# Optimization experiments

Hardware: AMD Instinct MI355X
Metric: run time of the kernel (lower is better)

## Reference

```python
import jax, jax.numpy as jnp
import numpy as np

H = 8        # num attention heads
DH = 160     # head dim (hidden_size // H)
HS = 1280    # hidden_size
CAD = 768    # cross_attention_dim
R = 4        # LoRA rank
LORA_SCALE = 1.0  # `scale` forward arg (default 1.0)


def setup_inputs() -> dict:
    key = jax.random.key(0)
    ks = jax.random.split(key, 16)
    rn = lambda k, s, std=0.02: (jax.random.normal(k, s) * std).astype(jnp.float32)
    return {
        "hidden_states": jax.random.normal(ks[0], (8, 4096, HS), jnp.float32),
        "encoder_hidden_states": jax.random.normal(ks[1], (8, 77, CAD), jnp.float32),
        # base attention projections (nn.Linear weight layout: [out, in])
        "Wq": rn(ks[2], (HS, HS)),
        "Wk": rn(ks[3], (HS, CAD)),
        "Wv": rn(ks[4], (HS, CAD)),
        "Wo": rn(ks[5], (HS, HS)),
        "bo": jnp.zeros((HS,), jnp.float32),
        # LoRA down/up pairs (down std ~ 1/rank; up nonzero so grads flow)
        "q_down": rn(ks[6], (R, HS), 0.25), "q_up": rn(ks[7], (HS, R)),
        "k_down": rn(ks[8], (R, CAD), 0.25), "k_up": rn(ks[9], (HS, R)),
        "v_down": rn(ks[10], (R, CAD), 0.25), "v_up": rn(ks[11], (HS, R)),
        "o_down": rn(ks[12], (R, HS), 0.25), "o_up": rn(ks[13], (HS, R)),
    }


def reference(hidden_states, encoder_hidden_states, Wq, Wk, Wv, Wo, bo,
              q_down, q_up, k_down, k_up, v_down, v_up, o_down, o_up):
    B, S, _ = hidden_states.shape
    T = encoder_hidden_states.shape[1]
    lora = lambda x, d, u: (x @ d.T) @ u.T  # LoRALinearLayer: up(down(x))

    q = hidden_states @ Wq.T + LORA_SCALE * lora(hidden_states, q_down, q_up)
    k = encoder_hidden_states @ Wk.T + LORA_SCALE * lora(encoder_hidden_states, k_down, k_up)
    v = encoder_hidden_states @ Wv.T + LORA_SCALE * lora(encoder_hidden_states, v_down, v_up)

    q = q.reshape(B, S, H, DH)
    k = k.reshape(B, T, H, DH)
    v = v.reshape(B, T, H, DH)

    # attn.get_attention_scores: scaled QK^T, softmax (no mask)
    inv_sqrt_d = jnp.asarray(1.0 / np.sqrt(DH), q.dtype)
    scores = jnp.einsum('bshd,bthd->bhst', q, k) * inv_sqrt_d
    probs = jax.nn.softmax(scores, axis=-1)
    o = jnp.einsum('bhst,bthd->bshd', probs, v).reshape(B, S, H * DH)

    # to_out[0] (Linear with bias) + LoRA on the same input; to_out[1] dropout = identity (eval)
    return o @ Wo.T + bo + LORA_SCALE * lora(o, o_down, o_up)
```

## Files before the change

### kernel.cpp

```cpp
#include <hip/hip_runtime.h>
#include <hip/hip_bf16.h>
#include <stdint.h>

typedef short bf16x8 __attribute__((ext_vector_type(8)));
typedef float f32x4 __attribute__((ext_vector_type(4)));

#define DEVI static __device__ __forceinline__

DEVI ushort f2bf(float f) {
  union { float f; uint32_t u; } v; v.f = f;
  uint32_t u = v.u;
  return (ushort)((u + 0x7fffu + ((u >> 16) & 1u)) >> 16);
}

DEVI void gload16(const void* g, void* l) {
  __builtin_amdgcn_global_load_lds((const __attribute__((address_space(1))) void*)g,
                                   (__attribute__((address_space(3))) void*)l,
                                   16, 0, 0);
}

#define SBAR() __builtin_amdgcn_sched_barrier(0)
#define KEY(r) (((r) & 3) ^ (((r) >> 2) & 3))


__global__ void fold_kernel(const float* __restrict__ W, const float* __restrict__ up,
                            const float* __restrict__ down, ushort* __restrict__ out,
                            int OUT, int IN, int transpose, float scale) {
  int idx = blockIdx.x * 256 + threadIdx.x;
  if (idx >= OUT * IN) return;
  int o = idx / IN, i = idx % IN;
  float v = W[idx];
#pragma unroll
  for (int r = 0; r < 4; ++r) v += up[o * 4 + r] * down[r * IN + i];
  v *= scale;
  out[transpose ? ((long)i * OUT + o) : idx] = f2bf(v);
}

__global__ void cvt_kernel(const float* __restrict__ in, ushort* __restrict__ out, int n8) {
  int idx = blockIdx.x * 256 + threadIdx.x;
  if (idx >= n8) return;
  const float4* p = (const float4*)(in + (long)idx * 8);
  float4 a = p[0], b = p[1];
  union { ushort us[8]; uint4 v; } r;
  r.us[0] = f2bf(a.x); r.us[1] = f2bf(a.y); r.us[2] = f2bf(a.z); r.us[3] = f2bf(a.w);
  r.us[4] = f2bf(b.x); r.us[5] = f2bf(b.y); r.us[6] = f2bf(b.z); r.us[7] = f2bf(b.w);
  *(uint4*)(out + (long)idx * 8) = r.v;
}


__global__ __launch_bounds__(256) void gemm_bt(
    const ushort* __restrict__ A, long sA0, long sA1, int lda, int validM,
    const ushort* __restrict__ B, long sB0, long sB1, int ldb, int validN,
    float* __restrict__ C32, ushort* __restrict__ C16, long sC0, long sC1, int ldc,
    const float* __restrict__ bias, int K)
{
  __shared__ ushort As[128 * 32];
  __shared__ ushort Bs[128 * 32];

  const int z = blockIdx.z;
  const ushort* Ab = A + (long)(z >> 3) * sA0 + (long)(z & 7) * sA1;
  const ushort* Bb = B + (long)(z >> 3) * sB0 + (long)(z & 7) * sB1;
  const int m0 = blockIdx.x * 128;
  const int n0 = blockIdx.y * 128;
  const int tid = threadIdx.x;
  const int lane = tid & 63;
  const int wid = tid >> 6;

  const int c0 = tid;
  const int arow0 = min(m0 + (c0 >> 2), validM - 1);
  const int arow1 = min(m0 + (c0 >> 2) + 64, validM - 1);
  const int brow0 = min(n0 + (c0 >> 2), validN - 1);
  const int brow1 = min(n0 + (c0 >> 2) + 64, validN - 1);
  const int seg = (c0 & 3) * 8;

  const int wr = (wid >> 1) * 64;
  const int wc = (wid & 1) * 64;
  const int frow = lane & 15;
  const int fk = (lane >> 4) * 8;

  f32x4 acc[4][4] = {};

  for (int kt = 0; kt < K; kt += 32) {
    gload16(Ab + (long)arow0 * lda + kt + seg, As + c0 * 8);
    gload16(Ab + (long)arow1 * lda + kt + seg, As + (c0 + 256) * 8);
    gload16(Bb + (long)brow0 * ldb + kt + seg, Bs + c0 * 8);
    gload16(Bb + (long)brow1 * ldb + kt + seg, Bs + (c0 + 256) * 8);
    __syncthreads();

    bf16x8 af[4], bfr[4];
#pragma unroll
    for (int m = 0; m < 4; ++m)
      af[m] = *(const bf16x8*)(As + (wr + m * 16 + frow) * 32 + fk);
#pragma unroll
    for (int n = 0; n < 4; ++n)
      bfr[n] = *(const bf16x8*)(Bs + (wc + n * 16 + frow) * 32 + fk);
#pragma unroll
    for (int m = 0; m < 4; ++m)
#pragma unroll
      for (int n = 0; n < 4; ++n)
        acc[m][n] = __builtin_amdgcn_mfma_f32_16x16x32_bf16(af[m], bfr[n], acc[m][n], 0, 0, 0);
    __syncthreads();
  }

  const long cb = (long)(z >> 3) * sC0 + (long)(z & 7) * sC1;
  const int crow = m0 + wr + (lane >> 4) * 4;
  const int ccol = n0 + wc + (lane & 15);
#pragma unroll
  for (int m = 0; m < 4; ++m)
#pragma unroll
    for (int n = 0; n < 4; ++n)
#pragma unroll
      for (int j = 0; j < 4; ++j) {
        int r = crow + m * 16 + j;
        int c = ccol + n * 16;
        if (r < validM && c < validN) {
          float v = acc[m][n][j];
          if (bias) v += bias[c];
          if (C32) C32[cb + (long)r * ldc + c] = v;
          else     C16[cb + (long)r * ldc + c] = f2bf(v);
        }
      }
}

__global__ __launch_bounds__(512, 2) void score_softmax(
    const float* __restrict__ hs, const ushort* __restrict__ Mt,
    ushort* __restrict__ probs)
{
  __shared__ ushort lds[45056];

  const int z = blockIdx.z;
  const int s0 = blockIdx.x * 256;
  const int h0 = blockIdx.y * 2;
  const int tid = threadIdx.x;
  const int lane = tid & 63;
  const int wid = tid >> 6;
  const int wM = wid >> 1;
  const int wN = wid & 1;

  const int arow = tid >> 1;
  const int akey = KEY(arow);
  const int sl0 = 2 * (tid & 1), sl1 = sl0 + 1;
  const float* ag = hs + ((long)z * 4096 + s0 + arow) * 1280;
  const int adst0 = arow * 32 + ((sl0 ^ akey) * 8);
  const int adst1 = arow * 32 + ((sl1 ^ akey) * 8);

  const int br1 = tid >> 2;
  const int br2 = 128 + (tid >> 2);
  const int bp = tid & 3;
  const ushort* MtB = Mt + (long)z * (640L * 1280);
  auto brow_src = [&](int rb) -> long {
    int hl = rb >= 96;
    int t = rb - 96 * hl;
    return (long)((h0 + hl) * 77 + min(t, 76)) * 1280;
  };
  const long bsrc1 = brow_src(br1) + ((bp ^ KEY(br1)) * 8);
  const long bsrc2 = brow_src(br2) + ((bp ^ KEY(br2)) * 8);
  const int bdst1 = tid * 8;
  const int bdst2 = 4096 + tid * 8;

  const int kk = lane >> 4;
  int afoff[4], bfoff[6];
#pragma unroll
  for (int m = 0; m < 4; ++m) {
    int r = wM * 64 + m * 16 + (lane & 15);
    afoff[m] = r * 32 + ((kk ^ KEY(r)) * 8);
  }
#pragma unroll
  for (int n = 0; n < 6; ++n) {
    int r = wN * 96 + n * 16 + (lane & 15);
    bfoff[n] = 8192 + r * 32 + ((kk ^ KEY(r)) * 8);
  }

  f32x4 acc[4][6] = {};
  const int NT = 40;

  {
    float4 pa0 = *(const float4*)(ag + sl0 * 8);
    float4 pa1 = *(const float4*)(ag + sl0 * 8 + 4);
    float4 pa2 = *(const float4*)(ag + sl1 * 8);
    float4 pa3 = *(const float4*)(ag + sl1 * 8 + 4);
    gload16(MtB + bsrc1, &lds[bdst1 + 8192]);
    if (tid < 256) gload16(MtB + bsrc2, &lds[bdst2 + 8192]);
    union { ushort us[8]; bf16x8 v; } c0, c1;
    c0.us[0]=f2bf(pa0.x); c0.us[1]=f2bf(pa0.y); c0.us[2]=f2bf(pa0.z); c0.us[3]=f2bf(pa0.w);
    c0.us[4]=f2bf(pa1.x); c0.us[5]=f2bf(pa1.y); c0.us[6]=f2bf(pa1.z); c0.us[7]=f2bf(pa1.w);
    c1.us[0]=f2bf(pa2.x); c1.us[1]=f2bf(pa2.y); c1.us[2]=f2bf(pa2.z); c1.us[3]=f2bf(pa2.w);
    c1.us[4]=f2bf(pa3.x); c1.us[5]=f2bf(pa3.y); c1.us[6]=f2bf(pa3.z); c1.us[7]=f2bf(pa3.w);
    *(bf16x8*)(&lds[adst0]) = c0.v;
    *(bf16x8*)(&lds[adst1]) = c1.v;
  }
  __syncthreads();

  for (int t = 0; t < NT; ++t) {
    const int cb = (t & 1) * 14336;
    const int nb = ((t & 1) ^ 1) * 14336;
    const bool pre = (t + 1 < NT);
    float4 pa0, pa1, pa2, pa3;
    if (pre) {
      const int k1 = (t + 1) * 32;
      pa0 = *(const float4*)(ag + k1 + sl0 * 8);
      pa1 = *(const float4*)(ag + k1 + sl0 * 8 + 4);
      pa2 = *(const float4*)(ag + k1 + sl1 * 8);
      pa3 = *(const float4*)(ag + k1 + sl1 * 8 + 4);
      gload16(MtB + k1 + bsrc1, &lds[nb + 8192 + bdst1]);
      if (tid < 256) gload16(MtB + k1 + bsrc2, &lds[nb + 8192 + bdst2]);
    }
    bf16x8 af[4], bfv[6];
#pragma unroll
    for (int m = 0; m < 4; ++m) af[m] = *(const bf16x8*)(&lds[cb + afoff[m]]);
#pragma unroll
    for (int n = 0; n < 6; ++n) bfv[n] = *(const bf16x8*)(&lds[cb + bfoff[n]]);
#pragma unroll
    for (int m = 0; m < 4; ++m)
#pragma unroll
      for (int n = 0; n < 6; ++n)
        acc[m][n] = __builtin_amdgcn_mfma_f32_16x16x32_bf16(af[m], bfv[n], acc[m][n], 0, 0, 0);
    if (pre) {
      union { ushort us[8]; bf16x8 v; } c0, c1;
      c0.us[0]=f2bf(pa0.x); c0.us[1]=f2bf(pa0.y); c0.us[2]=f2bf(pa0.z); c0.us[3]=f2bf(pa0.w);
      c0.us[4]=f2bf(pa1.x); c0.us[5]=f2bf(pa1.y); c0.us[6]=f2bf(pa1.z); c0.us[7]=f2bf(pa1.w);
      c1.us[0]=f2bf(pa2.x); c1.us[1]=f2bf(pa2.y); c1.us[2]=f2bf(pa2.z); c1.us[3]=f2bf(pa2.w);
      c1.us[4]=f2bf(pa3.x); c1.us[5]=f2bf(pa3.y); c1.us[6]=f2bf(pa3.z); c1.us[7]=f2bf(pa3.w);
      *(bf16x8*)(&lds[nb + adst0]) = c0.v;
      *(bf16x8*)(&lds[nb + adst1]) = c1.v;
    }
    __syncthreads();
  }

  const int l15 = lane & 15;
#pragma unroll
  for (int m = 0; m < 4; ++m)
#pragma unroll
    for (int j = 0; j < 4; ++j) {
      float mx = -1e30f;
#pragma unroll
      for (int n = 0; n < 6; ++n)
        if (n * 16 + l15 < 77) mx = fmaxf(mx, acc[m][n][j]);
#pragma unroll
      for (int o = 8; o; o >>= 1) mx = fmaxf(mx, __shfl_xor(mx, o));
      float sum = 0.f;
#pragma unroll
      for (int n = 0; n < 6; ++n) {
        float e = (n * 16 + l15 < 77) ? __expf(acc[m][n][j] - mx) : 0.f;
        acc[m][n][j] = e;
        sum += e;
      }
#pragma unroll
      for (int o = 8; o; o >>= 1) sum += __shfl_xor(sum, o);
      float inv = 1.f / sum;
#pragma unroll
      for (int n = 0; n < 6; ++n) acc[m][n][j] *= inv;
    }

  ushort* pw = lds + wid * 5632;
#pragma unroll
  for (int m = 0; m < 4; ++m)
#pragma unroll
    for (int n = 0; n < 5; ++n)
#pragma unroll
      for (int j = 0; j < 4; ++j)
        pw[(m * 16 + (lane >> 4) * 4 + j) * 88 + n * 16 + l15] = f2bf(acc[m][n][j]);

  const uint* pw32 = (const uint*)pw;
  uint* probs32 = (uint*)probs;
  const int head = h0 + wN;
  const long sbase = (long)z * 4096 + s0 + wM * 64;
#pragma unroll 4
  for (int k = 0; k < 40; ++k) {
    int f2 = k * 64 + lane;
    int r = f2 / 40;
    int tp = f2 - r * 40;
    probs32[(sbase + r) * 320 + head * 40 + tp] = pw32[r * 44 + tp];
  }
}

__global__ __launch_bounds__(512, 2) void gemm_out(
    const ushort* __restrict__ P, const ushort* __restrict__ Nt,
    float* __restrict__ C, const float* __restrict__ bias)
{
  __shared__ ushort lds[49152];

  const int z = blockIdx.z;
  const ushort* Ab = P + (long)z * (4096L * 640) + (long)blockIdx.x * 256 * 640;
  const ushort* Bb = Nt + (long)z * (1280L * 640) + (long)blockIdx.y * 128 * 640;
  const int tid = threadIdx.x;
  const int lane = tid & 63;
  const int wid = tid >> 6;
  const int wM = wid >> 2;
  const int wN = wid & 3;

  const int ar0 = tid >> 2;
  const int ar1 = 128 + (tid >> 2);
  const int ap = tid & 3;
  const long aoff0 = (long)ar0 * 640 + ((ap ^ KEY(ar0)) * 8);
  const long aoff1 = (long)ar1 * 640 + ((ap ^ KEY(ar1)) * 8);
  const int adst0 = tid * 8;
  const int adst1 = 4096 + tid * 8;
  const int brow = tid >> 2;
  const long boff = (long)brow * 640 + (((tid & 3) ^ KEY(brow)) * 8);
  const int bdst = 8192 + tid * 8;

  const int kk = lane >> 4;
  int afoff[8], bfoff[2];
#pragma unroll
  for (int m = 0; m < 8; ++m) {
    int r = wM * 128 + m * 16 + (lane & 15);
    afoff[m] = r * 32 + ((kk ^ KEY(r)) * 8);
  }
#pragma unroll
  for (int n = 0; n < 2; ++n) {
    int r = wN * 32 + n * 16 + (lane & 15);
    bfoff[n] = 8192 + r * 32 + ((kk ^ KEY(r)) * 8);
  }

  f32x4 acc[8][2] = {};
  const int NT = 20;

#define SA(tt)  { int sb = ((tt) & 3) * 12288; int pk = (tt) << 5; \
    gload16(Ab + aoff0 + pk, &lds[sb + adst0]); \
    gload16(Ab + aoff1 + pk, &lds[sb + adst1]); }
#define SBl(tt) { int sb = ((tt) & 3) * 12288; int pk = (tt) << 5; \
    gload16(Bb + boff + pk, &lds[sb + bdst]); }

  SA(0) SBl(0) SA(1) SBl(1) SA(2) SBl(2)
  asm volatile("s_waitcnt vmcnt(6)" ::: "memory");
  SBAR(); __builtin_amdgcn_s_barrier(); SBAR();

  for (int t = 0; t < NT; ++t) {
    const int base = (t & 3) * 12288;
    const bool pre = (t + 3 < NT);

    bf16x8 a0[4], a1[4], bv[2];
#pragma unroll
    for (int m = 0; m < 4; ++m) a0[m] = *(const bf16x8*)(&lds[base + afoff[m]]);
#pragma unroll
    for (int n = 0; n < 2; ++n) bv[n] = *(const bf16x8*)(&lds[base + bfoff[n]]);
    if (pre) SA(t + 3)
    SBAR(); __builtin_amdgcn_s_barrier(); SBAR();
    __builtin_amdgcn_s_setprio(1);
#pragma unroll
    for (int m = 0; m < 4; ++m)
#pragma unroll
      for (int n = 0; n < 2; ++n)
        acc[m][n] = __builtin_amdgcn_mfma_f32_16x16x32_bf16(a0[m], bv[n], acc[m][n], 0, 0, 0);
    __builtin_amdgcn_s_setprio(0);
    SBAR(); __builtin_amdgcn_s_barrier(); SBAR();

#pragma unroll
    for (int m = 0; m < 4; ++m) a1[m] = *(const bf16x8*)(&lds[base + afoff[m + 4]]);
    if (pre) SBl(t + 3)
    if (t + 3 < NT)      { asm volatile("s_waitcnt vmcnt(6)" ::: "memory"); }
    else if (t + 2 < NT) { asm volatile("s_waitcnt vmcnt(3)" ::: "memory"); }
    else                 { asm volatile("s_waitcnt vmcnt(0)" ::: "memory"); }
    SBAR(); __builtin_amdgcn_s_barrier(); SBAR();
    __builtin_amdgcn_s_setprio(1);
#pragma unroll
    for (int m = 4; m < 8; ++m)
#pragma unroll
      for (int n = 0; n < 2; ++n)
        acc[m][n] = __builtin_amdgcn_mfma_f32_16x16x32_bf16(a1[m - 4], bv[n], acc[m][n], 0, 0, 0);
    __builtin_amdgcn_s_setprio(0);
    SBAR(); __builtin_amdgcn_s_barrier(); SBAR();
  }
#undef SA
#undef SBl

  float* pw = (float*)lds + wid * 576;
  const int ccol = blockIdx.y * 128 + wN * 32;
  const float4 bv4 = *(const float4*)(bias + ccol + (lane & 7) * 4);
  const long crow0 = (long)z * 4096 + blockIdx.x * 256 + wM * 128;
#pragma unroll
  for (int m = 0; m < 8; ++m) {
#pragma unroll
    for (int n = 0; n < 2; ++n)
#pragma unroll
      for (int j = 0; j < 4; ++j)
        pw[((lane >> 4) * 4 + j) * 36 + n * 16 + (lane & 15)] = acc[m][n][j];
#pragma unroll
    for (int pass = 0; pass < 2; ++pass) {
      int r = pass * 8 + (lane >> 3);
      float4 v = *(const float4*)(pw + r * 36 + (lane & 7) * 4);
      v.x += bv4.x; v.y += bv4.y; v.z += bv4.z; v.w += bv4.w;
      *(float4*)(C + (crow0 + m * 16 + r) * 1280 + ccol + (lane & 7) * 4) = v;
    }
  }
}

__global__ void zero_nt_pad(ushort* __restrict__ Nt) {
  int idx = blockIdx.x * 256 + threadIdx.x;
  if (idx >= 8 * 1280 * 24) return;
  int b = idx / (1280 * 24);
  int rem = idx % (1280 * 24);
  int j = rem / 24, q = rem % 24;
  int h = q / 3, t = 77 + q % 3;
  Nt[(long)b * 1280 * 640 + (long)j * 640 + h * 80 + t] = 0;
}

extern "C" void kernel_launch(void* const* d_in, const int* in_sizes, int n_in,
                              void* d_out, int out_size, void* d_ws, size_t ws_size,
                              hipStream_t stream) {
  (void)in_sizes; (void)n_in; (void)out_size; (void)ws_size;
  const float* hs     = (const float*)d_in[0];
  const float* ehs    = (const float*)d_in[1];
  const float* Wq     = (const float*)d_in[2];
  const float* Wk     = (const float*)d_in[3];
  const float* Wv     = (const float*)d_in[4];
  const float* Wo     = (const float*)d_in[5];
  const float* bo     = (const float*)d_in[6];
  const float* q_down = (const float*)d_in[7];
  const float* q_up   = (const float*)d_in[8];
  const float* k_down = (const float*)d_in[9];
  const float* k_up   = (const float*)d_in[10];
  const float* v_down = (const float*)d_in[11];
  const float* v_up   = (const float*)d_in[12];
  const float* o_down = (const float*)d_in[13];
  const float* o_up   = (const float*)d_in[14];

  char* w = (char*)d_ws;
  size_t off = 0;
  auto alloc = [&](size_t b) { char* p = w + off; off = (off + b + 255) & ~(size_t)255; return p; };
  ushort* ehs_bf = (ushort*)alloc(616L * 768 * 2);
  ushort* WqT    = (ushort*)alloc(1280L * 1280 * 2);
  ushort* Wkv    = (ushort*)alloc(2560L * 768 * 2);
  ushort* Wo_bf  = (ushort*)alloc(1280L * 1280 * 2);
  ushort* kv_bf  = (ushort*)alloc(616L * 2560 * 2);
  ushort* Mt     = (ushort*)alloc(8L * 640 * 1280 * 2);
  ushort* Nt     = (ushort*)alloc(8L * 1280 * 640 * 2);
  ushort* probs  = (ushort*)alloc(8L * 4096 * 640 * 2);
  float*  outp   = (float*)d_out;
  const float invs = 0.07905694150420949f;

  fold_kernel<<<6400, 256, 0, stream>>>(Wq, q_up, q_down, WqT, 1280, 1280, 1, invs);
  fold_kernel<<<3840, 256, 0, stream>>>(Wk, k_up, k_down, Wkv, 1280, 768, 0, 1.0f);
  fold_kernel<<<3840, 256, 0, stream>>>(Wv, v_up, v_down, Wkv + 1280L * 768, 1280, 768, 0, 1.0f);
  fold_kernel<<<6400, 256, 0, stream>>>(Wo, o_up, o_down, Wo_bf, 1280, 1280, 0, 1.0f);
  cvt_kernel<<<231, 256, 0, stream>>>(ehs, ehs_bf, 59136);
  gemm_bt<<<dim3(5, 20, 1), 256, 0, stream>>>(ehs_bf, 0, 0, 768, 616,
      Wkv, 0, 0, 768, 2560, nullptr, kv_bf, 0, 0, 2560, nullptr, 768);
  gemm_bt<<<dim3(1, 10, 64), 256, 0, stream>>>(kv_bf, 77L * 2560, 160, 2560, 77,
      WqT, 0, 160, 1280, 1280, nullptr, Mt, 640L * 1280, 77L * 1280, 1280, nullptr, 160);
  gemm_bt<<<dim3(10, 1, 64), 256, 0, stream>>>(Wo_bf, 0, 160, 1280, 1280,
      kv_bf + 1280, 77L * 2560, 160, 2560, 77, nullptr, Nt, 1280L * 640, 80, 640, nullptr, 160);
  zero_nt_pad<<<960, 256, 0, stream>>>(Nt);
  score_softmax<<<dim3(16, 4, 8), 512, 0, stream>>>(hs, Mt, probs);
  gemm_out<<<dim3(16, 10, 8), 512, 0, stream>>>(probs, Nt, outp, bo);
}
```

Measured before the change: 347.6 us.

## Deepen K-step to 64 and restructure score/out GEMM pipelines with larger tiles

Both main kernels switch from 32-wide to 64-wide K stages with double-buffered LDS, an 8-way XOR swizzle, and explicit barrier/waitcnt phases that interleave MFMA groups with LDS reads and global prefetch. gemm_out widens its N tile from 128 to 256, halving grid.y and raising LDS use. Both kernels now run one block per CU. The aim is fewer barriers per FLOP and better reuse of A tiles, at the cost of occupancy and more registers.

New measurement: 362.5 us. 4.3% more time.

```diff
diff --git a/kernel.cpp b/kernel.cpp
--- a/kernel.cpp
+++ b/kernel.cpp
@@ -19,8 +19,11 @@
                                    16, 0, 0);
 }
 
-#define SBAR() __builtin_amdgcn_sched_barrier(0)
-#define KEY(r) (((r) & 3) ^ (((r) >> 2) & 3))
+#define SB() __builtin_amdgcn_sched_barrier(0)
+#define BAR() __builtin_amdgcn_s_barrier()
+#define LGK0() { asm volatile("s_waitcnt lgkmcnt(0)" ::: "memory"); SB(); }
+#define VM0()  { asm volatile("s_waitcnt vmcnt(0)" ::: "memory"); SB(); }
+#define MFMA(a, b, c) __builtin_amdgcn_mfma_f32_16x16x32_bf16((a), (b), (c), 0, 0, 0)
 
 
 __global__ void fold_kernel(const float* __restrict__ W, const float* __restrict__ up,
@@ -98,7 +101,7 @@
     for (int m = 0; m < 4; ++m)
 #pragma unroll
       for (int n = 0; n < 4; ++n)
-        acc[m][n] = __builtin_amdgcn_mfma_f32_16x16x32_bf16(af[m], bfr[n], acc[m][n], 0, 0, 0);
+        acc[m][n] = MFMA(af[m], bfr[n], acc[m][n]);
     __syncthreads();
   }
 
@@ -122,11 +125,11 @@
       }
 }
 
-__global__ __launch_bounds__(512, 2) void score_softmax(
+__global__ __launch_bounds__(512, 1) void score_softmax(
     const float* __restrict__ hs, const ushort* __restrict__ Mt,
     ushort* __restrict__ probs)
 {
-  __shared__ ushort lds[45056];
+  __shared__ ushort lds[57344];
 
   const int z = blockIdx.z;
   const int s0 = blockIdx.x * 256;
@@ -136,98 +139,121 @@
   const int wid = tid >> 6;
   const int wM = wid >> 1;
   const int wN = wid & 1;
-
-  const int arow = tid >> 1;
-  const int akey = KEY(arow);
-  const int sl0 = 2 * (tid & 1), sl1 = sl0 + 1;
-  const float* ag = hs + ((long)z * 4096 + s0 + arow) * 1280;
-  const int adst0 = arow * 32 + ((sl0 ^ akey) * 8);
-  const int adst1 = arow * 32 + ((sl1 ^ akey) * 8);
-
-  const int br1 = tid >> 2;
-  const int br2 = 128 + (tid >> 2);
-  const int bp = tid & 3;
+  const int l15 = lane & 15;
+  const int l4 = lane >> 4;
+
+  const int ar = tid >> 1, ah = tid & 1;
+  const float* ag = hs + ((long)z * 4096 + s0 + ar) * 1280 + ah * 32;
+  const int akey = ar & 7;
+  int awoff[4];
+#pragma unroll
+  for (int i = 0; i < 4; ++i) awoff[i] = ar * 64 + (((ah * 4 + i) ^ akey) * 8);
+
   const ushort* MtB = Mt + (long)z * (640L * 1280);
-  auto brow_src = [&](int rb) -> long {
-    int hl = rb >= 96;
-    int t = rb - 96 * hl;
-    return (long)((h0 + hl) * 77 + min(t, 76)) * 1280;
-  };
-  const long bsrc1 = brow_src(br1) + ((bp ^ KEY(br1)) * 8);
-  const long bsrc2 = brow_src(br2) + ((bp ^ KEY(br2)) * 8);
-  const int bdst1 = tid * 8;
-  const int bdst2 = 4096 + tid * 8;
-
-  const int kk = lane >> 4;
-  int afoff[4], bfoff[6];
-#pragma unroll
-  for (int m = 0; m < 4; ++m) {
-    int r = wM * 64 + m * 16 + (lane & 15);
-    afoff[m] = r * 32 + ((kk ^ KEY(r)) * 8);
-  }
-#pragma unroll
-  for (int n = 0; n < 6; ++n) {
-    int r = wN * 96 + n * 16 + (lane & 15);
-    bfoff[n] = 8192 + r * 32 + ((kk ^ KEY(r)) * 8);
+  const int rb0 = tid >> 3, sl = tid & 7;
+  long bsrc[3]; int bdst[3];
+#pragma unroll
+  for (int j = 0; j < 3; ++j) {
+    int rb = j * 64 + rb0;
+    int c = h0 * 96 + rb;
+    int hh = c / 96, tt = c - hh * 96;
+    tt = min(tt, 76);
+    bsrc[j] = (long)(hh * 77 + tt) * 1280 + ((sl ^ (rb & 7)) * 8);
+    bdst[j] = 16384 + j * 4096 + tid * 8;
+  }
+
+  int aoff[2][4], boff[2][6];
+#pragma unroll
+  for (int kk = 0; kk < 2; ++kk) {
+#pragma unroll
+    for (int m = 0; m < 4; ++m) {
+      int r = wM * 64 + m * 16 + l15;
+      aoff[kk][m] = r * 64 + (((kk * 4 + l4) ^ (r & 7)) * 8);
+    }
+#pragma unroll
+    for (int n = 0; n < 6; ++n) {
+      int r = wN * 96 + n * 16 + l15;
+      boff[kk][n] = 16384 + r * 64 + (((kk * 4 + l4) ^ (r & 7)) * 8);
+    }
   }
 
   f32x4 acc[4][6] = {};
-  const int NT = 40;
-
-  {
-    float4 pa0 = *(const float4*)(ag + sl0 * 8);
-    float4 pa1 = *(const float4*)(ag + sl0 * 8 + 4);
-    float4 pa2 = *(const float4*)(ag + sl1 * 8);
-    float4 pa3 = *(const float4*)(ag + sl1 * 8 + 4);
-    gload16(MtB + bsrc1, &lds[bdst1 + 8192]);
-    if (tid < 256) gload16(MtB + bsrc2, &lds[bdst2 + 8192]);
-    union { ushort us[8]; bf16x8 v; } c0, c1;
-    c0.us[0]=f2bf(pa0.x); c0.us[1]=f2bf(pa0.y); c0.us[2]=f2bf(pa0.z); c0.us[3]=f2bf(pa0.w);
-    c0.us[4]=f2bf(pa1.x); c0.us[5]=f2bf(pa1.y); c0.us[6]=f2bf(pa1.z); c0.us[7]=f2bf(pa1.w);
-    c1.us[0]=f2bf(pa2.x); c1.us[1]=f2bf(pa2.y); c1.us[2]=f2bf(pa2.z); c1.us[3]=f2bf(pa2.w);
-    c1.us[4]=f2bf(pa3.x); c1.us[5]=f2bf(pa3.y); c1.us[6]=f2bf(pa3.z); c1.us[7]=f2bf(pa3.w);
-    *(bf16x8*)(&lds[adst0]) = c0.v;
-    *(bf16x8*)(&lds[adst1]) = c1.v;
-  }
-  __syncthreads();
-
-  for (int t = 0; t < NT; ++t) {
-    const int cb = (t & 1) * 14336;
-    const int nb = ((t & 1) ^ 1) * 14336;
-    const bool pre = (t + 1 < NT);
-    float4 pa0, pa1, pa2, pa3;
-    if (pre) {
-      const int k1 = (t + 1) * 32;
-      pa0 = *(const float4*)(ag + k1 + sl0 * 8);
-      pa1 = *(const float4*)(ag + k1 + sl0 * 8 + 4);
-      pa2 = *(const float4*)(ag + k1 + sl1 * 8);
-      pa3 = *(const float4*)(ag + k1 + sl1 * 8 + 4);
-      gload16(MtB + k1 + bsrc1, &lds[nb + 8192 + bdst1]);
-      if (tid < 256) gload16(MtB + k1 + bsrc2, &lds[nb + 8192 + bdst2]);
-    }
-    bf16x8 af[4], bfv[6];
-#pragma unroll
-    for (int m = 0; m < 4; ++m) af[m] = *(const bf16x8*)(&lds[cb + afoff[m]]);
-#pragma unroll
-    for (int n = 0; n < 6; ++n) bfv[n] = *(const bf16x8*)(&lds[cb + bfoff[n]]);
-#pragma unroll
-    for (int m = 0; m < 4; ++m)
-#pragma unroll
-      for (int n = 0; n < 6; ++n)
-        acc[m][n] = __builtin_amdgcn_mfma_f32_16x16x32_bf16(af[m], bfv[n], acc[m][n], 0, 0, 0);
-    if (pre) {
-      union { ushort us[8]; bf16x8 v; } c0, c1;
-      c0.us[0]=f2bf(pa0.x); c0.us[1]=f2bf(pa0.y); c0.us[2]=f2bf(pa0.z); c0.us[3]=f2bf(pa0.w);
-      c0.us[4]=f2bf(pa1.x); c0.us[5]=f2bf(pa1.y); c0.us[6]=f2bf(pa1.z); c0.us[7]=f2bf(pa1.w);
-      c1.us[0]=f2bf(pa2.x); c1.us[1]=f2bf(pa2.y); c1.us[2]=f2bf(pa2.z); c1.us[3]=f2bf(pa2.w);
-      c1.us[4]=f2bf(pa3.x); c1.us[5]=f2bf(pa3.y); c1.us[6]=f2bf(pa3.z); c1.us[7]=f2bf(pa3.w);
-      *(bf16x8*)(&lds[nb + adst0]) = c0.v;
-      *(bf16x8*)(&lds[nb + adst1]) = c1.v;
-    }
-    __syncthreads();
-  }
-
-  const int l15 = lane & 15;
+  float4 af[8];
+
+#define SS_GLB(nb, kt) { \
+    gload16(MtB + bsrc[0] + (kt), &lds[(nb) + bdst[0]]); \
+    gload16(MtB + bsrc[1] + (kt), &lds[(nb) + bdst[1]]); \
+    gload16(MtB + bsrc[2] + (kt), &lds[(nb) + bdst[2]]); }
+#define SS_LOADA(kt) { _Pragma("unroll") \
+    for (int i = 0; i < 8; ++i) af[i] = *(const float4*)(ag + (kt) + i * 4); }
+#define SS_CVTW(nb) { \
+    union { ushort us[8]; bf16x8 v; } cw; \
+    _Pragma("unroll") \
+    for (int i = 0; i < 4; ++i) { \
+      float4 x = af[2 * i], y = af[2 * i + 1]; \
+      cw.us[0] = f2bf(x.x); cw.us[1] = f2bf(x.y); cw.us[2] = f2bf(x.z); cw.us[3] = f2bf(x.w); \
+      cw.us[4] = f2bf(y.x); cw.us[5] = f2bf(y.y); cw.us[6] = f2bf(y.z); cw.us[7] = f2bf(y.w); \
+      *(bf16x8*)(&lds[(nb) + awoff[i]]) = cw.v; \
+    } }
+#define SS_MF(MLO, KK, A0, A1) { \
+    __builtin_amdgcn_s_setprio(1); \
+    _Pragma("unroll") \
+    for (int n = 0; n < 6; ++n) { \
+      acc[MLO][n] = MFMA(A0, bfv[n], acc[MLO][n]); \
+      acc[MLO + 1][n] = MFMA(A1, bfv[n], acc[MLO + 1][n]); \
+    } \
+    __builtin_amdgcn_s_setprio(0); }
+
+  SS_GLB(0, 0)
+  SS_LOADA(0)
+  SS_CVTW(0)
+  VM0()
+  LGK0()
+  BAR(); SB();
+
+  for (int s = 0; s < 20; ++s) {
+    const int cb = (s & 1) * 28672;
+    const int nb = 28672 - cb;
+    const int kt1 = (s + 1) * 64;
+    const bool pre = (s + 1 < 20);
+    bf16x8 a0, a1, bfv[6];
+
+    a0 = *(const bf16x8*)(&lds[cb + aoff[0][0]]);
+    a1 = *(const bf16x8*)(&lds[cb + aoff[0][1]]);
+#pragma unroll
+    for (int n = 0; n < 6; ++n) bfv[n] = *(const bf16x8*)(&lds[cb + boff[0][n]]);
+    if (pre) { SS_GLB(nb, kt1) SS_LOADA(kt1) }
+    SB(); BAR();
+    LGK0()
+    SS_MF(0, 0, a0, a1)
+    SB(); BAR();
+
+    a0 = *(const bf16x8*)(&lds[cb + aoff[0][2]]);
+    a1 = *(const bf16x8*)(&lds[cb + aoff[0][3]]);
+    SB(); BAR();
+    LGK0()
+    SS_MF(2, 0, a0, a1)
+    SB(); BAR();
+
+    a0 = *(const bf16x8*)(&lds[cb + aoff[1][0]]);
+    a1 = *(const bf16x8*)(&lds[cb + aoff[1][1]]);
+#pragma unroll
+    for (int n = 0; n < 6; ++n) bfv[n] = *(const bf16x8*)(&lds[cb + boff[1][n]]);
+    SB(); BAR();
+    LGK0()
+    SS_MF(0, 1, a0, a1)
+    SB(); BAR();
+
+    a0 = *(const bf16x8*)(&lds[cb + aoff[1][2]]);
+    a1 = *(const bf16x8*)(&lds[cb + aoff[1][3]]);
+    if (pre) { SS_CVTW(nb) }
+    VM0()
+    SB(); BAR();
+    LGK0()
+    SS_MF(2, 1, a0, a1)
+    SB(); BAR();
+  }
+
 #pragma unroll
   for (int m = 0; m < 4; ++m)
 #pragma unroll
@@ -259,7 +285,7 @@
     for (int n = 0; n < 5; ++n)
 #pragma unroll
       for (int j = 0; j < 4; ++j)
-        pw[(m * 16 + (lane >> 4) * 4 + j) * 88 + n * 16 + l15] = f2bf(acc[m][n][j]);
+        pw[(m * 16 + l4 * 4 + j) * 88 + n * 16 + l15] = f2bf(acc[m][n][j]);
 
   const uint* pw32 = (const uint*)pw;
   uint* probs32 = (uint*)probs;
@@ -272,117 +298,141 @@
     int tp = f2 - r * 40;
     probs32[(sbase + r) * 320 + head * 40 + tp] = pw32[r * 44 + tp];
   }
-}
-
-__global__ __launch_bounds__(512, 2) void gemm_out(
+#undef SS_GLB
+#undef SS_LOADA
+#undef SS_CVTW
+#undef SS_MF
+}
+
+__global__ __launch_bounds__(512, 1) void gemm_out(
     const ushort* __restrict__ P, const ushort* __restrict__ Nt,
     float* __restrict__ C, const float* __restrict__ bias)
 {
-  __shared__ ushort lds[49152];
+  __shared__ ushort lds[65536];
 
   const int z = blockIdx.z;
   const ushort* Ab = P + (long)z * (4096L * 640) + (long)blockIdx.x * 256 * 640;
-  const ushort* Bb = Nt + (long)z * (1280L * 640) + (long)blockIdx.y * 128 * 640;
+  const ushort* Bb = Nt + (long)z * (1280L * 640) + (long)blockIdx.y * 256 * 640;
   const int tid = threadIdx.x;
   const int lane = tid & 63;
   const int wid = tid >> 6;
   const int wM = wid >> 2;
   const int wN = wid & 3;
-
-  const int ar0 = tid >> 2;
-  const int ar1 = 128 + (tid >> 2);
-  const int ap = tid & 3;
-  const long aoff0 = (long)ar0 * 640 + ((ap ^ KEY(ar0)) * 8);
-  const long aoff1 = (long)ar1 * 640 + ((ap ^ KEY(ar1)) * 8);
-  const int adst0 = tid * 8;
-  const int adst1 = 4096 + tid * 8;
-  const int brow = tid >> 2;
-  const long boff = (long)brow * 640 + (((tid & 3) ^ KEY(brow)) * 8);
-  const int bdst = 8192 + tid * 8;
-
-  const int kk = lane >> 4;
-  int afoff[8], bfoff[2];
+  const int l15 = lane & 15;
+  const int l4 = lane >> 4;
+
+  const int r0 = tid >> 3, sl = tid & 7;
+  long asrc[4], bsrc[4]; int adst[4], bdst[4];
+#pragma unroll
+  for (int j = 0; j < 4; ++j) {
+    int rr = j * 64 + r0;
+    asrc[j] = (long)rr * 640 + ((sl ^ (rr & 7)) * 8);
+    bsrc[j] = asrc[j];
+    adst[j] = j * 4096 + tid * 8;
+    bdst[j] = 16384 + j * 4096 + tid * 8;
+  }
+
+  int aoff[2][8], boff[2][4];
+#pragma unroll
+  for (int kk = 0; kk < 2; ++kk) {
+#pragma unroll
+    for (int m = 0; m < 8; ++m) {
+      int r = wM * 128 + m * 16 + l15;
+      aoff[kk][m] = r * 64 + (((kk * 4 + l4) ^ (r & 7)) * 8);
+    }
+#pragma unroll
+    for (int n = 0; n < 4; ++n) {
+      int r = wN * 64 + n * 16 + l15;
+      boff[kk][n] = 16384 + r * 64 + (((kk * 4 + l4) ^ (r & 7)) * 8);
+    }
+  }
+
+  f32x4 acc[8][4] = {};
+
+#define OG_STG(nb, kt, J0, J1) { \
+    gload16(Ab + asrc[J0] + (kt), &lds[(nb) + adst[J0]]); \
+    gload16(Ab + asrc[J1] + (kt), &lds[(nb) + adst[J1]]); \
+    gload16(Bb + bsrc[J0] + (kt), &lds[(nb) + bdst[J0]]); \
+    gload16(Bb + bsrc[J1] + (kt), &lds[(nb) + bdst[J1]]); }
+#define OG_MF(MLO) { \
+    __builtin_amdgcn_s_setprio(1); \
+    _Pragma("unroll") \
+    for (int q = 0; q < 4; ++q) \
+      _Pragma("unroll") \
+      for (int n = 0; n < 4; ++n) \
+        acc[(MLO) + q][n] = MFMA(av[q], bfv[n], acc[(MLO) + q][n]); \
+    __builtin_amdgcn_s_setprio(0); }
+
+  OG_STG(0, 0, 0, 1)
+  OG_STG(0, 0, 2, 3)
+  VM0()
+  BAR(); SB();
+
+  for (int s = 0; s < 10; ++s) {
+    const int cb = (s & 1) * 32768;
+    const int nb = 32768 - cb;
+    const int kt1 = (s + 1) * 64;
+    const bool pre = (s + 1 < 10);
+    bf16x8 av[4], bfv[4];
+
+#pragma unroll
+    for (int q = 0; q < 4; ++q) av[q] = *(const bf16x8*)(&lds[cb + aoff[0][q]]);
+#pragma unroll
+    for (int n = 0; n < 4; ++n) bfv[n] = *(const bf16x8*)(&lds[cb + boff[0][n]]);
+    if (pre) OG_STG(nb, kt1, 0, 1)
+    SB(); BAR();
+    LGK0()
+    OG_MF(0)
+    SB(); BAR();
+
+#pragma unroll
+    for (int q = 0; q < 4; ++q) av[q] = *(const bf16x8*)(&lds[cb + aoff[0][q + 4]]);
+    if (pre) OG_STG(nb, kt1, 2, 3)
+    SB(); BAR();
+    LGK0()
+    OG_MF(4)
+    SB(); BAR();
+
+#pragma unroll
+    for (int q = 0; q < 4; ++q) av[q] = *(const bf16x8*)(&lds[cb + aoff[1][q]]);
+#pragma unroll
+    for (int n = 0; n < 4; ++n) bfv[n] = *(const bf16x8*)(&lds[cb + boff[1][n]]);
+    SB(); BAR();
+    LGK0()
+    OG_MF(0)
+    SB(); BAR();
+
+#pragma unroll
+    for (int q = 0; q < 4; ++q) av[q] = *(const bf16x8*)(&lds[cb + aoff[1][q + 4]]);
+    VM0()
+    SB(); BAR();
+    LGK0()
+    OG_MF(4)
+    SB(); BAR();
+  }
+#undef OG_STG
+#undef OG_MF
+
+  float* pw = (float*)lds + wid * 1088;
+  const int ccol = blockIdx.y * 256 + wN * 64;
+  const float4 bv4 = *(const float4*)(bias + ccol + l15 * 4);
+  const long crow0 = (long)z * 4096 + blockIdx.x * 256 + wM * 128;
 #pragma unroll
   for (int m = 0; m < 8; ++m) {
-    int r = wM * 128 + m * 16 + (lane & 15);
-    afoff[m] = r * 32 + ((kk ^ KEY(r)) * 8);
-  }
-#pragma unroll
-  for (int n = 0; n < 2; ++n) {
-    int r = wN * 32 + n * 16 + (lane & 15);
-    bfoff[n] = 8192 + r * 32 + ((kk ^ KEY(r)) * 8);
-  }
-
-  f32x4 acc[8][2] = {};
-  const int NT = 20;
-
-#define SA(tt)  { int sb = ((tt) & 3) * 12288; int pk = (tt) << 5; \
-    gload16(Ab + aoff0 + pk, &lds[sb + adst0]); \
-    gload16(Ab + aoff1 + pk, &lds[sb + adst1]); }
-#define SBl(tt) { int sb = ((tt) & 3) * 12288; int pk = (tt) << 5; \
-    gload16(Bb + boff + pk, &lds[sb + bdst]); }
-
-  SA(0) SBl(0) SA(1) SBl(1) SA(2) SBl(2)
-  asm volatile("s_waitcnt vmcnt(6)" ::: "memory");
-  SBAR(); __builtin_amdgcn_s_barrier(); SBAR();
-
-  for (int t = 0; t < NT; ++t) {
-    const int base = (t & 3) * 12288;
-    const bool pre = (t + 3 < NT);
-
-    bf16x8 a0[4], a1[4], bv[2];
-#pragma unroll
-    for (int m = 0; m < 4; ++m) a0[m] = *(const bf16x8*)(&lds[base + afoff[m]]);
-#pragma unroll
-    for (int n = 0; n < 2; ++n) bv[n] = *(const bf16x8*)(&lds[base + bfoff[n]]);
-    if (pre) SA(t + 3)
-    SBAR(); __builtin_amdgcn_s_barrier(); SBAR();
-    __builtin_amdgcn_s_setprio(1);
-#pragma unroll
-    for (int m = 0; m < 4; ++m)
-#pragma unroll
-      for (int n = 0; n < 2; ++n)
-        acc[m][n] = __builtin_amdgcn_mfma_f32_16x16x32_bf16(a0[m], bv[n], acc[m][n], 0, 0, 0);
-    __builtin_amdgcn_s_setprio(0);
-    SBAR(); __builtin_amdgcn_s_barrier(); SBAR();
-
-#pragma unroll
-    for (int m = 0; m < 4; ++m) a1[m] = *(const bf16x8*)(&lds[base + afoff[m + 4]]);
-    if (pre) SBl(t + 3)
-    if (t + 3 < NT)      { asm volatile("s_waitcnt vmcnt(6)" ::: "memory"); }
-    else if (t + 2 < NT) { asm volatile("s_waitcnt vmcnt(3)" ::: "memory"); }
-    else                 { asm volatile("s_waitcnt vmcnt(0)" ::: "memory"); }
-    SBAR(); __builtin_amdgcn_s_barrier(); SBAR();
-    __builtin_amdgcn_s_setprio(1);
-#pragma unroll
-    for (int m = 4; m < 8; ++m)
-#pragma unroll
-      for (int n = 0; n < 2; ++n)
-        acc[m][n] = __builtin_amdgcn_mfma_f32_16x16x32_bf16(a1[m - 4], bv[n], acc[m][n], 0, 0, 0);
-    __builtin_amdgcn_s_setprio(0);
-    SBAR(); __builtin_amdgcn_s_barrier(); SBAR();
-  }
-#undef SA
-#undef SBl
-
-  float* pw = (float*)lds + wid * 576;
-  const int ccol = blockIdx.y * 128 + wN * 32;
-  const float4 bv4 = *(const float4*)(bias + ccol + (lane & 7) * 4);
-  const long crow0 = (long)z * 4096 + blockIdx.x * 256 + wM * 128;
-#pragma unroll
-  for (int m = 0; m < 8; ++m) {
-#pragma unroll
-    for (int n = 0; n < 2; ++n)
+#pragma unroll
+    for (int n = 0; n < 4; ++n)
 #pragma unroll
       for (int j = 0; j < 4; ++j)
-        pw[((lane >> 4) * 4 + j) * 36 + n * 16 + (lane & 15)] = acc[m][n][j];
-#pragma unroll
-    for (int pass = 0; pass < 2; ++pass) {
-      int r = pass * 8 + (lane >> 3);
-      float4 v = *(const float4*)(pw + r * 36 + (lane & 7) * 4);
+        pw[(l4 * 4 + j) * 68 + n * 16 + l15] = acc[m][n][j];
+    asm volatile("s_waitcnt lgkmcnt(0)" ::: "memory"); SB();
+#pragma unroll
+    for (int pass = 0; pass < 4; ++pass) {
+      int r = pass * 4 + l4;
+      float4 v = *(const float4*)(pw + r * 68 + l15 * 4);
       v.x += bv4.x; v.y += bv4.y; v.z += bv4.z; v.w += bv4.w;
-      *(float4*)(C + (crow0 + m * 16 + r) * 1280 + ccol + (lane & 7) * 4) = v;
-    }
+      *(float4*)(C + (crow0 + m * 16 + r) * 1280 + ccol + l15 * 4) = v;
+    }
+    asm volatile("s_waitcnt lgkmcnt(0)" ::: "memory"); SB();
   }
 }
 
@@ -443,5 +493,5 @@
       kv_bf + 1280, 77L * 2560, 160, 2560, 77, nullptr, Nt, 1280L * 640, 80, 640, nullptr, 160);
   zero_nt_pad<<<960, 256, 0, stream>>>(Nt);
   score_softmax<<<dim3(16, 4, 8), 512, 0, stream>>>(hs, Mt, probs);
-  gemm_out<<<dim3(16, 10, 8), 512, 0, stream>>>(probs, Nt, outp, bo);
-}
+  gemm_out<<<dim3(16, 5, 8), 512, 0, stream>>>(probs, Nt, outp, bo);
+}
```
